# Optimization experiments

Hardware: AMD Instinct MI355X
Metric: run time of the kernel (lower is better)

Reference implementation:

```python
import jax, jax.numpy as jnp
import numpy as np

H = 16          # num_heads
D = 1024        # in_features
NH = D // H     # per-head dim
EPS = 1e-5


def _ln(x, g, b):
    m = jnp.mean(x, axis=-1, keepdims=True)
    v = jnp.mean((x - m) ** 2, axis=-1, keepdims=True)
    return (x - m) / jnp.sqrt(v + EPS) * g + b


def _mha(q, k, v, Wq, bq, Wk, bk, Wv, bv, causal):
    # q: [Tq,B,D], k/v: [Tk,B,D]
    Tq, B, _ = q.shape
    Tk = k.shape[0]
    qh = (q @ Wq + bq).reshape(Tq, B, H, NH)
    kh = (k @ Wk + bk).reshape(Tk, B, H, NH)
    vh = (v @ Wv + bv).reshape(Tk, B, H, NH)
    scale = 1.0 / np.float32(np.sqrt(NH))
    logits = jnp.einsum('qbhd,kbhd->bhqk', qh, kh) * scale  # [B,H,Tq,Tk]
    if causal:
        mask = jnp.tril(jnp.ones((Tq, Tk), dtype=bool))
        logits = jnp.where(mask, logits, -jnp.inf)  # softmax over prefix [0..t]
    w = jax.nn.softmax(logits, axis=-1)
    out = jnp.einsum('bhqk,kbhd->qbhd', w, vh).reshape(Tq, B, D)
    return out


def setup_inputs() -> dict:
    key = jax.random.key(0)
    ks = jax.random.split(key, 12)
    s = 0.02
    T, B = 1024, 8
    inp = {
        'encoder_input': jax.random.normal(ks[0], (T, B, D), jnp.float32),
        'decoder_input': jax.random.normal(ks[1], (T, B, D), jnp.float32),
        # self-attention projections
        'Wq1': jax.random.normal(ks[2], (D, D), jnp.float32) * s,
        'bq1': jnp.zeros((D,), jnp.float32),
        'Wk1': jax.random.normal(ks[3], (D, D), jnp.float32) * s,
        'bk1': jnp.zeros((D,), jnp.float32),
        'Wv1': jax.random.normal(ks[4], (D, D), jnp.float32) * s,
        'bv1': jnp.zeros((D,), jnp.float32),
        # cross-attention projections
        'Wq2': jax.random.normal(ks[5], (D, D), jnp.float32) * s,
        'bq2': jnp.zeros((D,), jnp.float32),
        'Wk2': jax.random.normal(ks[6], (D, D), jnp.float32) * s,
        'bk2': jnp.zeros((D,), jnp.float32),
        'Wv2': jax.random.normal(ks[7], (D, D), jnp.float32) * s,
        'bv2': jnp.zeros((D,), jnp.float32),
        # position-wise linear
        'Wl': jax.random.normal(ks[8], (D, D), jnp.float32) * s,
        'bl': jnp.zeros((D,), jnp.float32),
        # layernorms
        'g1': jnp.ones((D,), jnp.float32), 'be1': jnp.zeros((D,), jnp.float32),
        'g2': jnp.ones((D,), jnp.float32), 'be2': jnp.zeros((D,), jnp.float32),
        'g3': jnp.ones((D,), jnp.float32), 'be3': jnp.zeros((D,), jnp.float32),
    }
    return inp


def reference(encoder_input, decoder_input,
              Wq1, bq1, Wk1, bk1, Wv1, bv1,
              Wq2, bq2, Wk2, bk2, Wv2, bv2,
              Wl, bl, g1, be1, g2, be2, g3, be3):
    # causal self-attention (prefix [:t+1] per step == causal mask)
    x = _mha(decoder_input, decoder_input, decoder_input,
             Wq1, bq1, Wk1, bk1, Wv1, bv1, causal=True)
    x = _ln(x + decoder_input, g1, be1)
    # cross-attention over full encoder input
    y = _mha(x, encoder_input, encoder_input,
             Wq2, bq2, Wk2, bk2, Wv2, bv2, causal=False)
    y = _ln(y + x, g2, be2)
    # position-wise linear (no activation in source) + residual + LN
    z = y @ Wl + bl
    out = _ln(z + y, g3, be3)
    return out
```

## Files before the change

kernel.cpp:

```cpp
#include <hip/hip_runtime.h>
#include <hip/hip_bf16.h>

typedef __bf16 bf16x8 __attribute__((ext_vector_type(8)));
typedef float f32x4 __attribute__((ext_vector_type(4)));

#define MFMA16(A, B, C) __builtin_amdgcn_mfma_f32_16x16x32_bf16(A, B, C, 0, 0, 0)

#define GLDS(gp, lp)                                                              \
    __builtin_amdgcn_global_load_lds(                                             \
        (const __attribute__((address_space(1))) void*)(gp),                      \
        (__attribute__((address_space(3))) void*)(lp), 16, 0, 0)

struct PtrW { const float* p[7]; };
__global__ __launch_bounds__(256) void wt_transpose(PtrW W, __hip_bfloat16* __restrict__ Wt) {
    const float* __restrict__ src = W.p[blockIdx.z];
    __hip_bfloat16* __restrict__ dst = Wt + ((size_t)blockIdx.z << 20);
    __shared__ float tile[32][33];
    const int bn = blockIdx.x * 32;
    const int bk = blockIdx.y * 32;
    const int tx = threadIdx.x, ty = threadIdx.y;
#pragma unroll
    for (int i = 0; i < 4; i++) {
        tile[ty + i * 8][tx] = src[(size_t)(bk + ty + i * 8) * 1024 + bn + tx];
    }
    __syncthreads();
#pragma unroll
    for (int i = 0; i < 4; i++) {
        dst[(size_t)(bn + ty + i * 8) * 1024 + bk + tx] =
            __float2bfloat16(tile[tx][ty + i * 8]);
    }
}

struct PtrC { const float* s[2]; __hip_bfloat16* d[2]; };
__global__ __launch_bounds__(256) void to_bf16(PtrC c) {
    const int z = blockIdx.y;
    const int i = (blockIdx.x * 256 + threadIdx.x) * 4;
    const float4 v = *(const float4*)(c.s[z] + i);
    __align__(8) __hip_bfloat16 t[4] = {__float2bfloat16(v.x), __float2bfloat16(v.y),
                                        __float2bfloat16(v.z), __float2bfloat16(v.w)};
    *(uint2*)(c.d[z] + i) = *(const uint2*)t;
}

struct Ptr5 { const float* p[5]; };
__global__ __launch_bounds__(256) void bias_concat(Ptr5 srcs, float* __restrict__ dst) {
    const int i = threadIdx.x * 4;
    *(float4*)(dst + blockIdx.x * 1024 + i) = *(const float4*)(srcs.p[blockIdx.x] + i);
}

__global__ __launch_bounds__(256) void v_transpose(const __hip_bfloat16* __restrict__ src,
                                                   __hip_bfloat16* __restrict__ Vt,
                                                   int S, int coloff) {
    __shared__ __hip_bfloat16 tile[64][72];
    const int t0 = blockIdx.x * 64;
    const int bh = blockIdx.y;
    const int b = bh & 7, h = bh >> 3;
    const int tid = threadIdx.x;
    const int r = tid >> 2, c = (tid & 3) * 16;
    const __hip_bfloat16* sp =
        src + (size_t)((t0 + r) * 8 + b) * S + coloff + h * 64 + c;
    *(uint4*)(&tile[r][c]) = *(const uint4*)(sp);
    *(uint4*)(&tile[r][c + 8]) = *(const uint4*)(sp + 8);
    __syncthreads();
    const int d = tid >> 2, tc = (tid & 3) * 16;
    __align__(16) __hip_bfloat16 tmp[16];
#pragma unroll
    for (int j = 0; j < 16; j++) tmp[j] = tile[tc + j][d];
    __hip_bfloat16* op = Vt + ((size_t)(b * 16 + h) << 16) + (size_t)d * 1024 + t0 + tc;
    *(uint4*)(op) = *(const uint4*)(tmp);
    *(uint4*)(op + 8) = *(const uint4*)(tmp + 8);
}

__global__ __launch_bounds__(256) void gemm_bias_kernel(
    const __hip_bfloat16* __restrict__ A, const __hip_bfloat16* __restrict__ Bt,
    const float* __restrict__ bias, float* __restrict__ Cf,
    __hip_bfloat16* __restrict__ Cb, int M, int N, int K,
    float qscale, int qcols) {
    __shared__ __align__(16) __hip_bfloat16 As[2][128 * 32];
    __shared__ __align__(16) __hip_bfloat16 Bs[2][128 * 32];
    const int tid = threadIdx.x;
    const int wave = tid >> 6, lane = tid & 63;
    const int quad = lane >> 4, l16 = lane & 15;
    const int m0 = blockIdx.x * 128, n0 = blockIdx.y * 128;
    const int wm = (wave & 1) * 64, wn = (wave >> 1) * 64;
    const int srow = lane >> 2;
    const int lc = (lane & 3) ^ ((lane >> 3) & 3);
    const __hip_bfloat16* ap[2];
    const __hip_bfloat16* bp[2];
    int loff[2];
#pragma unroll
    for (int u = 0; u < 2; u++) {
        const int g = wave * 2 + u;
        const int row = g * 16 + srow;
        ap[u] = A + (size_t)(m0 + row) * K + lc * 8;
        bp[u] = Bt + (size_t)(n0 + row) * K + lc * 8;
        loff[u] = g * 512;
    }
    const int pch = quad ^ ((l16 >> 1) & 3);
    f32x4 acc[4][4] = {};
#pragma unroll
    for (int u = 0; u < 2; u++) {
        GLDS(ap[u], &As[0][loff[u]]);
        GLDS(bp[u], &Bs[0][loff[u]]);
    }
    int sel = 0;
    for (int k0 = 0; k0 < K; k0 += 32) {
        __syncthreads();
        if (k0 + 32 < K) {
#pragma unroll
            for (int u = 0; u < 2; u++) {
                GLDS(ap[u] + k0 + 32, &As[sel ^ 1][loff[u]]);
                GLDS(bp[u] + k0 + 32, &Bs[sel ^ 1][loff[u]]);
            }
        }
        bf16x8 af[4], bfr[4];
#pragma unroll
        for (int i = 0; i < 4; i++) {
            af[i] = *(const bf16x8*)(&As[sel][(wm + i * 16 + l16) * 32 + pch * 8]);
            bfr[i] = *(const bf16x8*)(&Bs[sel][(wn + i * 16 + l16) * 32 + pch * 8]);
        }
#pragma unroll
        for (int i = 0; i < 4; i++)
#pragma unroll
            for (int j = 0; j < 4; j++)
                acc[i][j] = MFMA16(af[i], bfr[j], acc[i][j]);
        sel ^= 1;
    }
#pragma unroll
    for (int i = 0; i < 4; i++) {
#pragma unroll
        for (int j = 0; j < 4; j++) {
            const int mr = m0 + wm + i * 16 + quad * 4;
            const int nc = n0 + wn + j * 16 + l16;
            const float sc = (nc < qcols) ? qscale : 1.0f;
            const float bv = bias[nc];
#pragma unroll
            for (int r = 0; r < 4; r++) {
                const float v = (acc[i][j][r] + bv) * sc;
                const size_t idx = (size_t)(mr + r) * N + nc;
                if (Cf) Cf[idx] = v;
                if (Cb) Cb[idx] = __float2bfloat16(v);
            }
        }
    }
}

__global__ __launch_bounds__(256) void attn_kernel(
    const __hip_bfloat16* __restrict__ Qp, const __hip_bfloat16* __restrict__ Kp,
    const __hip_bfloat16* __restrict__ Vt, __hip_bfloat16* __restrict__ Ob,
    int T, int qRS, int kRS, int causal) {
    __shared__ __align__(16) __hip_bfloat16 Ks[2][64 * 64];
    __shared__ __align__(16) __hip_bfloat16 Vs[2][64 * 64];
    __shared__ __align__(16) __hip_bfloat16 Ps[4][16 * 64];
    const int tid = threadIdx.x, wave = tid >> 6, lane = tid & 63;
    const int quad = lane >> 4, l16 = lane & 15;
    const int gid = blockIdx.x;
    const int bh = (gid & 7) * 16 + ((gid >> 3) & 15);
    const int qt = gid >> 7;
    const int b = bh & 7, h = bh >> 3;
    const int q0 = qt * 128;
    const int qstride = 8 * qRS, kstride = 8 * kRS;
    const int sw = l16 & 7;

    const int qg0 = q0 + wave * 16;
    const int qg1 = qg0 + 64;
    const int myq0 = qg0 + l16, myq1 = qg1 + l16;
    const __hip_bfloat16* qbase = Qp + (size_t)b * qRS + h * 64;
    const bf16x8 qf00 = *(const bf16x8*)(qbase + (size_t)myq0 * qstride + quad * 8);
    const bf16x8 qf01 = *(const bf16x8*)(qbase + (size_t)myq0 * qstride + 32 + quad * 8);
    const bf16x8 qf10 = *(const bf16x8*)(qbase + (size_t)myq1 * qstride + quad * 8);
    const bf16x8 qf11 = *(const bf16x8*)(qbase + (size_t)myq1 * qstride + 32 + quad * 8);
    bf16x8 onesf;
#pragma unroll
    for (int i = 0; i < 8; i++) onesf[i] = (__bf16)1.0f;

    const int jk = wave * 2;
    const int lrow = lane >> 3;
    const int lch = (lane & 7) ^ (lrow & 7);
    const __hip_bfloat16* kp0 =
        Kp + (size_t)b * kRS + h * 64 + (size_t)(jk * 8 + lrow) * kstride + lch * 8;
    const __hip_bfloat16* kp1 = kp0 + (size_t)8 * kstride;
    const __hip_bfloat16* vp0 =
        Vt + ((size_t)(b * 16 + h) << 16) + (size_t)(jk * 8 + lrow) * 1024 + lch * 8;
    const __hip_bfloat16* vp1 = vp0 + 8 * 1024;
    const size_t kinc = (size_t)64 * kstride;

    f32x4 o0[4] = {}, o1[4] = {};
    f32x4 ol0 = {}, ol1 = {};
    bf16x8 pf00, pf01, pf10, pf11;

    auto softmax = [&](f32x4* s, f32x4& ol, bf16x8& pf0, bf16x8& pf1, int qg, int myq,
                       int k0) {
        const bool nm = causal && (k0 + 63 > qg);
        if (nm) {
#pragma unroll
            for (int n = 0; n < 4; n++)
#pragma unroll
                for (int r = 0; r < 4; r++)
                    if (k0 + n * 16 + quad * 4 + r > myq) s[n][r] = -1e30f;
        }
#pragma unroll
        for (int n = 0; n < 4; n++) {
            const float p0 = __builtin_amdgcn_exp2f(s[n][0]);
            const float p1 = __builtin_amdgcn_exp2f(s[n][1]);
            const float p2 = __builtin_amdgcn_exp2f(s[n][2]);
            const float p3 = __builtin_amdgcn_exp2f(s[n][3]);
            const __hip_bfloat162 pa = __float22bfloat162_rn(make_float2(p0, p1));
            const __hip_bfloat162 pb = __float22bfloat162_rn(make_float2(p2, p3));
            uint2 w;
            w.x = *(const unsigned int*)&pa;
            w.y = *(const unsigned int*)&pb;
            const int gcp = 2 * n + (quad >> 1);
            *(uint2*)(&Ps[wave][l16 * 64 + ((gcp ^ sw) << 3) + (quad & 1) * 4]) = w;
        }
        pf0 = *(const bf16x8*)(&Ps[wave][l16 * 64 + ((quad ^ sw) << 3)]);
        pf1 = *(const bf16x8*)(&Ps[wave][l16 * 64 + (((quad + 4) ^ sw) << 3)]);
        ol = MFMA16(onesf, pf0, ol);
        ol = MFMA16(onesf, pf1, ol);
    };

    const int kend = causal ? (q0 + 128) : T;
    GLDS(kp0, &Ks[0][jk * 512]);
    GLDS(kp1, &Ks[0][jk * 512 + 512]);
    GLDS(vp0, &Vs[0][jk * 512]);
    GLDS(vp1, &Vs[0][jk * 512 + 512]);
    const __hip_bfloat16* kn0 = kp0 + kinc;
    const __hip_bfloat16* kn1 = kp1 + kinc;
    const __hip_bfloat16* vn0 = vp0 + 64;
    const __hip_bfloat16* vn1 = vp1 + 64;
    int sel = 0;
    for (int k0 = 0; k0 < kend; k0 += 64) {
        __syncthreads();
        if (k0 + 64 < kend) {
            GLDS(kn0, &Ks[sel ^ 1][jk * 512]);
            GLDS(kn1, &Ks[sel ^ 1][jk * 512 + 512]);
            GLDS(vn0, &Vs[sel ^ 1][jk * 512]);
            GLDS(vn1, &Vs[sel ^ 1][jk * 512 + 512]);
            kn0 += kinc; kn1 += kinc; vn0 += 64; vn1 += 64;
        }
        const bool act0 = !causal || (k0 <= qg0 + 15);
        f32x4 s0[4] = {}, s1[4] = {};
        {
            bf16x8 kf[4];
#pragma unroll
            for (int n = 0; n < 4; n++)
                kf[n] = *(const bf16x8*)(&Ks[sel][(n * 16 + l16) * 64 +
                                                  ((quad ^ sw) << 3)]);
#pragma unroll
            for (int n = 0; n < 4; n++) {
                if (act0) s0[n] = MFMA16(kf[n], qf00, s0[n]);
                s1[n] = MFMA16(kf[n], qf10, s1[n]);
            }
#pragma unroll
            for (int n = 0; n < 4; n++)
                kf[n] = *(const bf16x8*)(&Ks[sel][(n * 16 + l16) * 64 +
                                                  (((quad + 4) ^ sw) << 3)]);
#pragma unroll
            for (int n = 0; n < 4; n++) {
                if (act0) s0[n] = MFMA16(kf[n], qf01, s0[n]);
                s1[n] = MFMA16(kf[n], qf11, s1[n]);
            }
        }
        if (act0) softmax(s0, ol0, pf00, pf01, qg0, myq0, k0);
        softmax(s1, ol1, pf10, pf11, qg1, myq1, k0);
#pragma unroll
        for (int mm = 0; mm < 4; mm++) {
            const int vrow = (mm * 16 + l16) * 64;
            const bf16x8 vf0 = *(const bf16x8*)(&Vs[sel][vrow + ((quad ^ sw) << 3)]);
            const bf16x8 vf1 = *(const bf16x8*)(&Vs[sel][vrow + (((quad + 4) ^ sw) << 3)]);
            if (act0) {
                o0[mm] = MFMA16(vf0, pf00, o0[mm]);
                o0[mm] = MFMA16(vf1, pf01, o0[mm]);
            }
            o1[mm] = MFMA16(vf0, pf10, o1[mm]);
            o1[mm] = MFMA16(vf1, pf11, o1[mm]);
        }
        sel ^= 1;
    }
    const float inv0 = 1.0f / ol0[0];
    const float inv1 = 1.0f / ol1[0];
    __hip_bfloat16* ob0 = Ob + (size_t)b * 1024 + h * 64 + (size_t)myq0 * 8192;
    __hip_bfloat16* ob1 = Ob + (size_t)b * 1024 + h * 64 + (size_t)myq1 * 8192;
#pragma unroll
    for (int mm = 0; mm < 4; mm++) {
        __align__(8) __hip_bfloat16 t0[4] = {
            __float2bfloat16(o0[mm][0] * inv0), __float2bfloat16(o0[mm][1] * inv0),
            __float2bfloat16(o0[mm][2] * inv0), __float2bfloat16(o0[mm][3] * inv0)};
        *(uint2*)(ob0 + mm * 16 + quad * 4) = *(const uint2*)t0;
        __align__(8) __hip_bfloat16 t1[4] = {
            __float2bfloat16(o1[mm][0] * inv1), __float2bfloat16(o1[mm][1] * inv1),
            __float2bfloat16(o1[mm][2] * inv1), __float2bfloat16(o1[mm][3] * inv1)};
        *(uint2*)(ob1 + mm * 16 + quad * 4) = *(const uint2*)t1;
    }
}

__global__ __launch_bounds__(256) void ln_res_kernel(
    const __hip_bfloat16* __restrict__ a, const float* __restrict__ bres,
    const float* __restrict__ g, const float* __restrict__ be,
    float* __restrict__ outf, __hip_bfloat16* __restrict__ outb) {
    const int row = blockIdx.x;
    const int tid = threadIdx.x;
    const size_t off = (size_t)row * 1024 + tid * 4;
    uint2 ar = *(const uint2*)(a + off);
    const __hip_bfloat16* ah = (const __hip_bfloat16*)&ar;
    const float4 vb = *(const float4*)(bres + off);
    float x0 = __bfloat162float(ah[0]) + vb.x;
    float x1 = __bfloat162float(ah[1]) + vb.y;
    float x2 = __bfloat162float(ah[2]) + vb.z;
    float x3 = __bfloat162float(ah[3]) + vb.w;
    float s = x0 + x1 + x2 + x3;
    float ss = x0 * x0 + x1 * x1 + x2 * x2 + x3 * x3;
#pragma unroll
    for (int w = 32; w >= 1; w >>= 1) {
        s += __shfl_xor(s, w);
        ss += __shfl_xor(ss, w);
    }
    __shared__ float sm[4], sv[4];
    const int wave = tid >> 6;
    if ((tid & 63) == 0) { sm[wave] = s; sv[wave] = ss; }
    __syncthreads();
    s = sm[0] + sm[1] + sm[2] + sm[3];
    ss = sv[0] + sv[1] + sv[2] + sv[3];
    const float mean = s * (1.f / 1024.f);
    const float inv = rsqrtf(ss * (1.f / 1024.f) - mean * mean + 1e-5f);
    const float4 gg = *(const float4*)(g + tid * 4);
    const float4 bb = *(const float4*)(be + tid * 4);
    const float y0 = (x0 - mean) * inv * gg.x + bb.x;
    const float y1 = (x1 - mean) * inv * gg.y + bb.y;
    const float y2 = (x2 - mean) * inv * gg.z + bb.z;
    const float y3 = (x3 - mean) * inv * gg.w + bb.w;
    if (outf) *(float4*)(outf + off) = make_float4(y0, y1, y2, y3);
    if (outb) {
        __align__(8) __hip_bfloat16 t[4] = {__float2bfloat16(y0), __float2bfloat16(y1),
                                            __float2bfloat16(y2), __float2bfloat16(y3)};
        *(uint2*)(outb + off) = *(const uint2*)t;
    }
}

extern "C" void kernel_launch(void* const* d_in, const int* in_sizes, int n_in,
                              void* d_out, int out_size, void* d_ws, size_t ws_size,
                              hipStream_t stream) {
    const float* enc = (const float*)d_in[0];
    const float* dec = (const float*)d_in[1];
    const float* Wq1 = (const float*)d_in[2];
    const float* bq1 = (const float*)d_in[3];
    const float* Wk1 = (const float*)d_in[4];
    const float* bk1 = (const float*)d_in[5];
    const float* Wv1 = (const float*)d_in[6];
    const float* bv1 = (const float*)d_in[7];
    const float* Wq2 = (const float*)d_in[8];
    const float* bq2 = (const float*)d_in[9];
    const float* Wk2 = (const float*)d_in[10];
    const float* bk2 = (const float*)d_in[11];
    const float* Wv2 = (const float*)d_in[12];
    const float* bv2 = (const float*)d_in[13];
    const float* Wl = (const float*)d_in[14];
    const float* bl = (const float*)d_in[15];
    const float* g1 = (const float*)d_in[16];
    const float* be1 = (const float*)d_in[17];
    const float* g2 = (const float*)d_in[18];
    const float* be2 = (const float*)d_in[19];
    const float* g3 = (const float*)d_in[20];
    const float* be3 = (const float*)d_in[21];
    float* outp = (float*)d_out;

    char* p = (char*)d_ws;
    auto alloc = [&](size_t n) {
        char* r = p;
        p += (n + 255) & ~(size_t)255;
        return r;
    };
    const size_t MD = (size_t)8192 * 1024;
    __hip_bfloat16* enc_b = (__hip_bfloat16*)alloc(MD * 2);
    __hip_bfloat16* dec_b = (__hip_bfloat16*)alloc(MD * 2);
    __hip_bfloat16* Wt = (__hip_bfloat16*)alloc((size_t)7 * 1024 * 1024 * 2);
    float* bcat = (float*)alloc((3072 + 2048) * sizeof(float));
    __hip_bfloat16* qkv = (__hip_bfloat16*)alloc(MD * 3 * 2);
    __hip_bfloat16* qb = (__hip_bfloat16*)alloc(MD * 2);
    __hip_bfloat16* attnb = (__hip_bfloat16*)alloc(MD * 2);
    __hip_bfloat16* Vtb = (__hip_bfloat16*)alloc(MD * 2);
    float* xf = (float*)alloc(MD * 4);
    float* yf = (float*)alloc(MD * 4);
    __hip_bfloat16* xb = dec_b;
    __hip_bfloat16* yb = enc_b;

    const float QSC = 0.18033688f;

    PtrW wptrs = {{Wq1, Wk1, Wv1, Wq2, Wk2, Wv2, Wl}};
    wt_transpose<<<dim3(32, 32, 7), dim3(32, 8), 0, stream>>>(wptrs, Wt);
    PtrC cp = {{enc, dec}, {enc_b, dec_b}};
    to_bf16<<<dim3(8192, 2), 256, 0, stream>>>(cp);
    Ptr5 bp = {{bq1, bk1, bv1, bk2, bv2}};
    bias_concat<<<5, 256, 0, stream>>>(bp, bcat);

    gemm_bias_kernel<<<dim3(64, 24), 256, 0, stream>>>(dec_b, Wt, bcat, nullptr, qkv,
                                                       8192, 3072, 1024, QSC, 1024);
    v_transpose<<<dim3(16, 128), 256, 0, stream>>>(qkv, Vtb, 3072, 2048);
    attn_kernel<<<1024, 256, 0, stream>>>(qkv, qkv + 1024, Vtb, attnb,
                                          1024, 3072, 3072, 1);
    ln_res_kernel<<<8192, 256, 0, stream>>>(attnb, dec, g1, be1, xf, xb);

    gemm_bias_kernel<<<dim3(64, 8), 256, 0, stream>>>(
        xb, Wt + (size_t)3 * 1024 * 1024, bq2, nullptr, qb, 8192, 1024, 1024, QSC, 1024);
    gemm_bias_kernel<<<dim3(64, 16), 256, 0, stream>>>(
        enc_b, Wt + (size_t)4 * 1024 * 1024, bcat + 3072, nullptr, qkv, 8192, 2048, 1024,
        1.0f, 0);
    v_transpose<<<dim3(16, 128), 256, 0, stream>>>(qkv, Vtb, 2048, 1024);
    attn_kernel<<<1024, 256, 0, stream>>>(qb, qkv, Vtb, attnb, 1024, 1024, 2048, 0);
    ln_res_kernel<<<8192, 256, 0, stream>>>(attnb, xf, g2, be2, yf, yb);

    gemm_bias_kernel<<<dim3(64, 8), 256, 0, stream>>>(
        yb, Wt + (size_t)6 * 1024 * 1024, bl, nullptr, qb, 8192, 1024, 1024, 1.0f, 0);
    ln_res_kernel<<<8192, 256, 0, stream>>>(qb, yf, g3, be3, outp, nullptr);
}
```

Measured before the change: 531.7 us.

## Compute V transposed directly in GEMM, drop fp32 residuals, wave-per-row layernorm

Adds a GEMM that computes V^T = Wv^T·X per batch and writes it straight into the per-head transposed layout. This removes the separate V projection output and the v_transpose passes. LayerNorm now handles one row per wave, so the cross-wave shared-memory reduction and barrier are gone, and the residuals for LN2 and LN3 are read from bf16 copies instead of the fp32 buffers. Causal attention blocks are launched heaviest-first (reversed q-tile order) to improve tail balance. Using bf16 residuals lowers precision, and the Vt GEMM's scattered 2-byte stores may be less efficient.

```diff
diff --git a/kernel.cpp b/kernel.cpp
--- a/kernel.cpp
+++ b/kernel.cpp
@@ -41,33 +41,10 @@
     *(uint2*)(c.d[z] + i) = *(const uint2*)t;
 }
 
-struct Ptr5 { const float* p[5]; };
-__global__ __launch_bounds__(256) void bias_concat(Ptr5 srcs, float* __restrict__ dst) {
+struct Ptr2 { const float* p[2]; };
+__global__ __launch_bounds__(256) void bias_concat(Ptr2 srcs, float* __restrict__ dst) {
     const int i = threadIdx.x * 4;
     *(float4*)(dst + blockIdx.x * 1024 + i) = *(const float4*)(srcs.p[blockIdx.x] + i);
-}
-
-__global__ __launch_bounds__(256) void v_transpose(const __hip_bfloat16* __restrict__ src,
-                                                   __hip_bfloat16* __restrict__ Vt,
-                                                   int S, int coloff) {
-    __shared__ __hip_bfloat16 tile[64][72];
-    const int t0 = blockIdx.x * 64;
-    const int bh = blockIdx.y;
-    const int b = bh & 7, h = bh >> 3;
-    const int tid = threadIdx.x;
-    const int r = tid >> 2, c = (tid & 3) * 16;
-    const __hip_bfloat16* sp =
-        src + (size_t)((t0 + r) * 8 + b) * S + coloff + h * 64 + c;
-    *(uint4*)(&tile[r][c]) = *(const uint4*)(sp);
-    *(uint4*)(&tile[r][c + 8]) = *(const uint4*)(sp + 8);
-    __syncthreads();
-    const int d = tid >> 2, tc = (tid & 3) * 16;
-    __align__(16) __hip_bfloat16 tmp[16];
-#pragma unroll
-    for (int j = 0; j < 16; j++) tmp[j] = tile[tc + j][d];
-    __hip_bfloat16* op = Vt + ((size_t)(b * 16 + h) << 16) + (size_t)d * 1024 + t0 + tc;
-    *(uint4*)(op) = *(const uint4*)(tmp);
-    *(uint4*)(op + 8) = *(const uint4*)(tmp + 8);
 }
 
 __global__ __launch_bounds__(256) void gemm_bias_kernel(
@@ -144,6 +121,80 @@
     }
 }
 
+__global__ __launch_bounds__(256) void gemm_vt_kernel(
+    const __hip_bfloat16* __restrict__ A, const __hip_bfloat16* __restrict__ X,
+    const float* __restrict__ bias, __hip_bfloat16* __restrict__ Vt) {
+    __shared__ __align__(16) __hip_bfloat16 As[2][128 * 32];
+    __shared__ __align__(16) __hip_bfloat16 Bs[2][128 * 32];
+    const int tid = threadIdx.x;
+    const int wave = tid >> 6, lane = tid & 63;
+    const int quad = lane >> 4, l16 = lane & 15;
+    const int m0 = blockIdx.x * 128, n0 = blockIdx.y * 128;
+    const int bb = blockIdx.z;
+    const int wm = (wave & 1) * 64, wn = (wave >> 1) * 64;
+    const int srow = lane >> 2;
+    const int lc = (lane & 3) ^ ((lane >> 3) & 3);
+    const __hip_bfloat16* ap[2];
+    const __hip_bfloat16* bp[2];
+    int loff[2];
+#pragma unroll
+    for (int u = 0; u < 2; u++) {
+        const int g = wave * 2 + u;
+        const int row = g * 16 + srow;
+        ap[u] = A + (size_t)(m0 + row) * 1024 + lc * 8;
+        bp[u] = X + ((size_t)(n0 + row) * 8 + bb) * 1024 + lc * 8;
+        loff[u] = g * 512;
+    }
+    const int pch = quad ^ ((l16 >> 1) & 3);
+    f32x4 acc[4][4] = {};
+#pragma unroll
+    for (int u = 0; u < 2; u++) {
+        GLDS(ap[u], &As[0][loff[u]]);
+        GLDS(bp[u], &Bs[0][loff[u]]);
+    }
+    int sel = 0;
+    for (int k0 = 0; k0 < 1024; k0 += 32) {
+        __syncthreads();
+        if (k0 + 32 < 1024) {
+#pragma unroll
+            for (int u = 0; u < 2; u++) {
+                GLDS(ap[u] + k0 + 32, &As[sel ^ 1][loff[u]]);
+                GLDS(bp[u] + k0 + 32, &Bs[sel ^ 1][loff[u]]);
+            }
+        }
+        bf16x8 af[4], bfr[4];
+#pragma unroll
+        for (int i = 0; i < 4; i++) {
+            af[i] = *(const bf16x8*)(&As[sel][(wm + i * 16 + l16) * 32 + pch * 8]);
+            bfr[i] = *(const bf16x8*)(&Bs[sel][(wn + i * 16 + l16) * 32 + pch * 8]);
+        }
+#pragma unroll
+        for (int i = 0; i < 4; i++)
+#pragma unroll
+            for (int j = 0; j < 4; j++)
+                acc[i][j] = MFMA16(af[i], bfr[j], acc[i][j]);
+        sel ^= 1;
+    }
+#pragma unroll
+    for (int i = 0; i < 4; i++) {
+        const int mr = m0 + wm + i * 16 + quad * 4;
+        float bias_r[4];
+#pragma unroll
+        for (int r = 0; r < 4; r++) bias_r[r] = bias[mr + r];
+#pragma unroll
+        for (int j = 0; j < 4; j++) {
+            const int nc = n0 + wn + j * 16 + l16;
+#pragma unroll
+            for (int r = 0; r < 4; r++) {
+                const int d = mr + r;
+                const size_t idx = ((size_t)bb << 20) + ((size_t)(d >> 6) << 16) +
+                                   (size_t)(d & 63) * 1024 + nc;
+                Vt[idx] = __float2bfloat16(acc[i][j][r] + bias_r[r]);
+            }
+        }
+    }
+}
+
 __global__ __launch_bounds__(256) void attn_kernel(
     const __hip_bfloat16* __restrict__ Qp, const __hip_bfloat16* __restrict__ Kp,
     const __hip_bfloat16* __restrict__ Vt, __hip_bfloat16* __restrict__ Ob,
@@ -155,7 +206,7 @@
     const int quad = lane >> 4, l16 = lane & 15;
     const int gid = blockIdx.x;
     const int bh = (gid & 7) * 16 + ((gid >> 3) & 15);
-    const int qt = gid >> 7;
+    const int qt = 7 - (gid >> 7);
     const int b = bh & 7, h = bh >> 3;
     const int q0 = qt * 128;
     const int qstride = 8 * qRS, kstride = 8 * kRS;
@@ -294,45 +345,63 @@
 }
 
 __global__ __launch_bounds__(256) void ln_res_kernel(
-    const __hip_bfloat16* __restrict__ a, const float* __restrict__ bres,
-    const float* __restrict__ g, const float* __restrict__ be,
-    float* __restrict__ outf, __hip_bfloat16* __restrict__ outb) {
-    const int row = blockIdx.x;
-    const int tid = threadIdx.x;
-    const size_t off = (size_t)row * 1024 + tid * 4;
-    uint2 ar = *(const uint2*)(a + off);
-    const __hip_bfloat16* ah = (const __hip_bfloat16*)&ar;
-    const float4 vb = *(const float4*)(bres + off);
-    float x0 = __bfloat162float(ah[0]) + vb.x;
-    float x1 = __bfloat162float(ah[1]) + vb.y;
-    float x2 = __bfloat162float(ah[2]) + vb.z;
-    float x3 = __bfloat162float(ah[3]) + vb.w;
-    float s = x0 + x1 + x2 + x3;
-    float ss = x0 * x0 + x1 * x1 + x2 * x2 + x3 * x3;
+    const __hip_bfloat16* __restrict__ a, const float* __restrict__ resf,
+    const __hip_bfloat16* __restrict__ resb, const float* __restrict__ g,
+    const float* __restrict__ be, float* __restrict__ outf,
+    __hip_bfloat16* __restrict__ outb) {
+    const int tid = threadIdx.x, wave = tid >> 6, lane = tid & 63;
+    const int row = blockIdx.x * 4 + wave;
+    const size_t base = (size_t)row * 1024;
+    float x[16];
+#pragma unroll
+    for (int c = 0; c < 4; c++) {
+        const int off = c * 256 + lane * 4;
+        const uint2 ar = *(const uint2*)(a + base + off);
+        const __hip_bfloat16* ah = (const __hip_bfloat16*)&ar;
+        if (resf) {
+            const float4 rv = *(const float4*)(resf + base + off);
+            x[c * 4 + 0] = __bfloat162float(ah[0]) + rv.x;
+            x[c * 4 + 1] = __bfloat162float(ah[1]) + rv.y;
+            x[c * 4 + 2] = __bfloat162float(ah[2]) + rv.z;
+            x[c * 4 + 3] = __bfloat162float(ah[3]) + rv.w;
+        } else {
+            const uint2 br = *(const uint2*)(resb + base + off);
+            const __hip_bfloat16* bhp = (const __hip_bfloat16*)&br;
+#pragma unroll
+            for (int k = 0; k < 4; k++)
+                x[c * 4 + k] = __bfloat162float(ah[k]) + __bfloat162float(bhp[k]);
+        }
+    }
+    float s = 0.f, ss = 0.f;
+#pragma unroll
+    for (int k = 0; k < 16; k++) {
+        s += x[k];
+        ss += x[k] * x[k];
+    }
 #pragma unroll
     for (int w = 32; w >= 1; w >>= 1) {
         s += __shfl_xor(s, w);
         ss += __shfl_xor(ss, w);
     }
-    __shared__ float sm[4], sv[4];
-    const int wave = tid >> 6;
-    if ((tid & 63) == 0) { sm[wave] = s; sv[wave] = ss; }
-    __syncthreads();
-    s = sm[0] + sm[1] + sm[2] + sm[3];
-    ss = sv[0] + sv[1] + sv[2] + sv[3];
     const float mean = s * (1.f / 1024.f);
     const float inv = rsqrtf(ss * (1.f / 1024.f) - mean * mean + 1e-5f);
-    const float4 gg = *(const float4*)(g + tid * 4);
-    const float4 bb = *(const float4*)(be + tid * 4);
-    const float y0 = (x0 - mean) * inv * gg.x + bb.x;
-    const float y1 = (x1 - mean) * inv * gg.y + bb.y;
-    const float y2 = (x2 - mean) * inv * gg.z + bb.z;
-    const float y3 = (x3 - mean) * inv * gg.w + bb.w;
-    if (outf) *(float4*)(outf + off) = make_float4(y0, y1, y2, y3);
-    if (outb) {
-        __align__(8) __hip_bfloat16 t[4] = {__float2bfloat16(y0), __float2bfloat16(y1),
-                                            __float2bfloat16(y2), __float2bfloat16(y3)};
-        *(uint2*)(outb + off) = *(const uint2*)t;
+#pragma unroll
+    for (int c = 0; c < 4; c++) {
+        const int off = c * 256 + lane * 4;
+        const float4 gg = *(const float4*)(g + off);
+        const float4 bb = *(const float4*)(be + off);
+        float y[4];
+        y[0] = (x[c * 4 + 0] - mean) * inv * gg.x + bb.x;
+        y[1] = (x[c * 4 + 1] - mean) * inv * gg.y + bb.y;
+        y[2] = (x[c * 4 + 2] - mean) * inv * gg.z + bb.z;
+        y[3] = (x[c * 4 + 3] - mean) * inv * gg.w + bb.w;
+        if (outf) *(float4*)(outf + base + off) = make_float4(y[0], y[1], y[2], y[3]);
+        if (outb) {
+            __align__(8) __hip_bfloat16 t[4] = {
+                __float2bfloat16(y[0]), __float2bfloat16(y[1]),
+                __float2bfloat16(y[2]), __float2bfloat16(y[3])};
+            *(uint2*)(outb + base + off) = *(const uint2*)t;
+        }
     }
 }
 
@@ -373,13 +442,11 @@
     __hip_bfloat16* enc_b = (__hip_bfloat16*)alloc(MD * 2);
     __hip_bfloat16* dec_b = (__hip_bfloat16*)alloc(MD * 2);
     __hip_bfloat16* Wt = (__hip_bfloat16*)alloc((size_t)7 * 1024 * 1024 * 2);
-    float* bcat = (float*)alloc((3072 + 2048) * sizeof(float));
-    __hip_bfloat16* qkv = (__hip_bfloat16*)alloc(MD * 3 * 2);
+    float* bcat = (float*)alloc(2048 * sizeof(float));
+    __hip_bfloat16* qk = (__hip_bfloat16*)alloc(MD * 2 * 2);
     __hip_bfloat16* qb = (__hip_bfloat16*)alloc(MD * 2);
     __hip_bfloat16* attnb = (__hip_bfloat16*)alloc(MD * 2);
     __hip_bfloat16* Vtb = (__hip_bfloat16*)alloc(MD * 2);
-    float* xf = (float*)alloc(MD * 4);
-    float* yf = (float*)alloc(MD * 4);
     __hip_bfloat16* xb = dec_b;
     __hip_bfloat16* yb = enc_b;
 
@@ -389,26 +456,27 @@
     wt_transpose<<<dim3(32, 32, 7), dim3(32, 8), 0, stream>>>(wptrs, Wt);
     PtrC cp = {{enc, dec}, {enc_b, dec_b}};
     to_bf16<<<dim3(8192, 2), 256, 0, stream>>>(cp);
-    Ptr5 bp = {{bq1, bk1, bv1, bk2, bv2}};
-    bias_concat<<<5, 256, 0, stream>>>(bp, bcat);
-
-    gemm_bias_kernel<<<dim3(64, 24), 256, 0, stream>>>(dec_b, Wt, bcat, nullptr, qkv,
-                                                       8192, 3072, 1024, QSC, 1024);
-    v_transpose<<<dim3(16, 128), 256, 0, stream>>>(qkv, Vtb, 3072, 2048);
-    attn_kernel<<<1024, 256, 0, stream>>>(qkv, qkv + 1024, Vtb, attnb,
-                                          1024, 3072, 3072, 1);
-    ln_res_kernel<<<8192, 256, 0, stream>>>(attnb, dec, g1, be1, xf, xb);
+    Ptr2 bp = {{bq1, bk1}};
+    bias_concat<<<2, 256, 0, stream>>>(bp, bcat);
+
+    gemm_bias_kernel<<<dim3(64, 16), 256, 0, stream>>>(dec_b, Wt, bcat, nullptr, qk,
+                                                       8192, 2048, 1024, QSC, 1024);
+    gemm_vt_kernel<<<dim3(8, 8, 8), 256, 0, stream>>>(Wt + (size_t)2 * 1024 * 1024,
+                                                      dec_b, bv1, Vtb);
+    attn_kernel<<<1024, 256, 0, stream>>>(qk, qk + 1024, Vtb, attnb,
+                                          1024, 2048, 2048, 1);
+    ln_res_kernel<<<2048, 256, 0, stream>>>(attnb, dec, nullptr, g1, be1, nullptr, xb);
 
     gemm_bias_kernel<<<dim3(64, 8), 256, 0, stream>>>(
         xb, Wt + (size_t)3 * 1024 * 1024, bq2, nullptr, qb, 8192, 1024, 1024, QSC, 1024);
-    gemm_bias_kernel<<<dim3(64, 16), 256, 0, stream>>>(
-        enc_b, Wt + (size_t)4 * 1024 * 1024, bcat + 3072, nullptr, qkv, 8192, 2048, 1024,
-        1.0f, 0);
-    v_transpose<<<dim3(16, 128), 256, 0, stream>>>(qkv, Vtb, 2048, 1024);
-    attn_kernel<<<1024, 256, 0, stream>>>(qb, qkv, Vtb, attnb, 1024, 1024, 2048, 0);
-    ln_res_kernel<<<8192, 256, 0, stream>>>(attnb, xf, g2, be2, yf, yb);
+    gemm_bias_kernel<<<dim3(64, 8), 256, 0, stream>>>(
+        enc_b, Wt + (size_t)4 * 1024 * 1024, bk2, nullptr, qk, 8192, 1024, 1024, 1.0f, 0);
+    gemm_vt_kernel<<<dim3(8, 8, 8), 256, 0, stream>>>(Wt + (size_t)5 * 1024 * 1024,
+                                                      enc_b, bv2, Vtb);
+    attn_kernel<<<1024, 256, 0, stream>>>(qb, qk, Vtb, attnb, 1024, 1024, 1024, 0);
+    ln_res_kernel<<<2048, 256, 0, stream>>>(attnb, nullptr, xb, g2, be2, nullptr, yb);
 
     gemm_bias_kernel<<<dim3(64, 8), 256, 0, stream>>>(
         yb, Wt + (size_t)6 * 1024 * 1024, bl, nullptr, qb, 8192, 1024, 1024, 1.0f, 0);
-    ln_res_kernel<<<8192, 256, 0, stream>>>(qb, yf, g3, be3, outp, nullptr);
-}
+    ln_res_kernel<<<2048, 256, 0, stream>>>(qb, nullptr, yb, g3, be3, outp, nullptr);
+}
```

Result: faster. 514.6 us (-3.2%).
